# Kernel optimization log

Hardware: AMD Instinct MI355X
Metric: run time of the kernel (lower is better)

The kernel has to match this reference:

```python
import jax, jax.numpy as jnp
import numpy as np

HEADS = 8
DIM_HEAD = 64
SCALE = DIM_HEAD ** -0.5


def setup_inputs() -> dict:
    key = jax.random.key(0)
    ks = jax.random.split(key, 5)
    dim, hidden = 512, HEADS * DIM_HEAD
    b, l = 4, 2048
    return {
        "x": jax.random.normal(ks[0], (b, dim, l), jnp.float32),
        "w_qkv": jax.random.normal(ks[1], (3 * hidden, dim), jnp.float32) * 0.02,
        "b_qkv": jax.random.normal(ks[2], (3 * hidden,), jnp.float32) * 0.02,
        "w_out": jax.random.normal(ks[3], (dim, hidden), jnp.float32) * 0.02,
        "b_out": jax.random.normal(ks[4], (dim,), jnp.float32) * 0.02,
    }


def reference(x, w_qkv, b_qkv, w_out, b_out):
    b, c, l = x.shape
    # Conv1d kernel-size-1 == per-position linear: (b, 3*hidden, l)
    qkv = jnp.einsum('oc,bcl->bol', w_qkv, x) + b_qkv[None, :, None]
    q, k, v = jnp.split(qkv, 3, axis=1)
    # rearrange 'b (h d) l -> b h d l'
    def split_heads(t):
        return t.reshape(b, HEADS, DIM_HEAD, l)
    q, k, v = split_heads(q) * SCALE, split_heads(k), split_heads(v)
    sim = jnp.einsum('bhdi,bhdj->bhij', q, k)  # [b,h,l,l]
    sim = sim - jax.lax.stop_gradient(jnp.max(sim, axis=-1, keepdims=True))
    attn = jax.nn.softmax(sim, axis=-1)
    out = jnp.einsum('bhij,bhdj->bhid', attn, v)  # [b,h,l,d]
    # 'b h l d -> b (h d) l'
    out = out.transpose(0, 1, 3, 2).reshape(b, HEADS * DIM_HEAD, l)
    out = jnp.einsum('oc,bcl->bol', w_out, out) + b_out[None, :, None]
    return out
```

## Files before the change

kernel.cpp:

```cpp
#include <hip/hip_runtime.h>
#include <hip/hip_bf16.h>

#define B 4
#define DIM 512
#define HID 512
#define NH 8
#define DH 64
#define L 2048
#define SCALE 0.125f

typedef __attribute__((ext_vector_type(8)))  short bf16x8;
typedef __attribute__((ext_vector_type(4)))  float f32x4;
typedef __attribute__((ext_vector_type(16))) float f32x16;
typedef __attribute__((ext_vector_type(4)))  int   i32x4;

static __device__ __forceinline__ short f32_to_bf16s(float f) {
    __hip_bfloat16 h = __float2bfloat16(f);
    return *reinterpret_cast<short*>(&h);
}
static __device__ __forceinline__ float bf16s_to_f32(short s) {
    return __uint_as_float(((unsigned)(unsigned short)s) << 16);
}

static __device__ __forceinline__ void gl_lds16(const short* g, short* l) {
    __builtin_amdgcn_global_load_lds(
        (const __attribute__((address_space(1))) void*)g,
        (__attribute__((address_space(3))) void*)l, 16, 0, 0);
}

static __device__ __forceinline__ bf16x8 lds_frag(const short* t, int row, int c) {
    bf16x8 v;
    __builtin_memcpy(&v, t + row * 64 + ((c ^ (row & 7)) * 8), 16);
    return v;
}

__global__ __launch_bounds__(256) void prep_w(
    const float* __restrict__ wq, const float* __restrict__ wo,
    short* __restrict__ dst)
{
    const int g = blockIdx.x * 256 + threadIdx.x;
    const int i = g * 4;
    float4 v;
    if (i < 786432) v = *(const float4*)(wq + i);
    else            v = *(const float4*)(wo + (i - 786432));
    short4 pk = {f32_to_bf16s(v.x), f32_to_bf16s(v.y),
                 f32_to_bf16s(v.z), f32_to_bf16s(v.w)};
    *(short4*)(dst + i) = pk;
}

__global__ __launch_bounds__(256) void transpose_x(
    const float* __restrict__ X, short* __restrict__ XT)
{
    const int l0 = blockIdx.x * 64;
    const int c0 = blockIdx.y * 64;
    const int b  = blockIdx.z;
    const int tid = threadIdx.x;

    __shared__ float tile[64][65];
    const float* Xb = X + (size_t)b * DIM * L;

    #pragma unroll
    for (int it = 0; it < 16; ++it) {
        const int cr = (tid >> 6) + it * 4;
        const int lc = tid & 63;
        tile[cr][lc] = Xb[(size_t)(c0 + cr) * L + l0 + lc];
    }
    __syncthreads();
    short* XTb = XT + (size_t)b * L * DIM;
    #pragma unroll
    for (int it = 0; it < 8; ++it) {
        const int l  = (tid >> 5) + it * 8;
        const int c2 = (tid & 31) * 2;
        short2 pk = {f32_to_bf16s(tile[c2][l]), f32_to_bf16s(tile[c2 + 1][l])};
        *(short2*)(XTb + (size_t)(l0 + l) * DIM + c0 + c2) = pk;
    }
}

__global__ __launch_bounds__(256) void qkv_mfma(
    const short* __restrict__ Wb, const short* __restrict__ XT,
    const float* __restrict__ bias,
    short* __restrict__ qws, short* __restrict__ kws, short* __restrict__ vws)
{
    const int lBase = blockIdx.x * 128;
    const int oBase = blockIdx.y * 128;
    const int b     = blockIdx.z;
    const int tid   = threadIdx.x;
    const int wave  = tid >> 6;
    const int lane  = tid & 63;
    const int lid   = lane & 15;
    const int quad  = lane >> 4;
    const int rsub  = lane >> 3;
    const int cl    = (lane & 7) ^ rsub;

    __shared__ __align__(16) short Wt[128 * 64];
    __shared__ __align__(16) short Xt[128 * 64];

    const short* XTb = XT + (size_t)b * L * DIM;
    const int oLoc = (wave & 1) * 64;
    const int lLoc = (wave >> 1) * 64;

    f32x4 acc[4][4];
    #pragma unroll
    for (int mi = 0; mi < 4; ++mi)
        #pragma unroll
        for (int ni = 0; ni < 4; ++ni) acc[mi][ni] = (f32x4){0.f, 0.f, 0.f, 0.f};

    for (int c0 = 0; c0 < DIM; c0 += 64) {
        if (c0) __syncthreads();
        #pragma unroll
        for (int t = 0; t < 4; ++t) {
            const int ch = wave * 4 + t;
            const int r  = ch * 8 + rsub;
            gl_lds16(Wb  + (size_t)(oBase + r) * DIM + c0 + cl * 8, Wt + ch * 512);
            gl_lds16(XTb + (size_t)(lBase + r) * DIM + c0 + cl * 8, Xt + ch * 512);
        }
        __syncthreads();
        #pragma unroll
        for (int kc = 0; kc < 2; ++kc) {
            bf16x8 a[4], bb[4];
            #pragma unroll
            for (int mi = 0; mi < 4; ++mi)
                a[mi] = lds_frag(Wt, oLoc + mi * 16 + lid, kc * 4 + quad);
            #pragma unroll
            for (int ni = 0; ni < 4; ++ni)
                bb[ni] = lds_frag(Xt, lLoc + ni * 16 + lid, kc * 4 + quad);
            #pragma unroll
            for (int mi = 0; mi < 4; ++mi)
                #pragma unroll
                for (int ni = 0; ni < 4; ++ni)
                    acc[mi][ni] = __builtin_amdgcn_mfma_f32_16x16x32_bf16(
                        a[mi], bb[ni], acc[mi][ni], 0, 0, 0);
        }
    }

    const int rty = oBase >> 9;
    const float sc = (rty == 0) ? SCALE : 1.0f;
    const int h = ((oBase + oLoc) >> 6) & 7;

    #pragma unroll
    for (int mi = 0; mi < 4; ++mi) {
        const int dB = mi * 16 + quad * 4;
        float bia[4];
        #pragma unroll
        for (int r = 0; r < 4; ++r)
            bia[r] = bias[oBase + oLoc + mi * 16 + quad * 4 + r];

        if (rty < 2) {
            short* dst = (rty == 0 ? qws : kws) + (((size_t)b * NH + h) * L) * DH;
            #pragma unroll
            for (int ni = 0; ni < 4; ++ni) {
                const int l = lBase + lLoc + ni * 16 + lid;
                short4 pk = {f32_to_bf16s((acc[mi][ni][0] + bia[0]) * sc),
                             f32_to_bf16s((acc[mi][ni][1] + bia[1]) * sc),
                             f32_to_bf16s((acc[mi][ni][2] + bia[2]) * sc),
                             f32_to_bf16s((acc[mi][ni][3] + bia[3]) * sc)};
                *(short4*)(dst + (size_t)l * DH + dB) = pk;
            }
        } else {
            short* dst = vws + (((size_t)b * NH + h) * DH) * L;
            #pragma unroll
            for (int r = 0; r < 4; ++r) {
                const int d = dB + r;
                #pragma unroll
                for (int ni = 0; ni < 4; ++ni)
                    dst[(size_t)d * L + lBase + lLoc + ni * 16 + lid] =
                        f32_to_bf16s((acc[mi][ni][r] + bia[r]) * sc);
            }
        }
    }
}

__global__ __launch_bounds__(256) void attn_mfma(
    const short* __restrict__ Q, const short* __restrict__ K,
    const short* __restrict__ VT,
    float* __restrict__ Op0, float* __restrict__ Op1,
    float* __restrict__ Lp0, float* __restrict__ Lp1)
{
    const int iTile = blockIdx.x;
    const int h     = blockIdx.y;
    const int b     = blockIdx.z >> 1;
    const int half  = blockIdx.z & 1;
    const int tid   = threadIdx.x;
    const int wave  = tid >> 6;
    const int lane  = tid & 63;
    const int l5    = lane & 31;
    const int me    = lane >> 5;
    const int rsub  = lane >> 3;
    const int cl    = (lane & 7) ^ rsub;

    float* __restrict__ Op = half ? Op1 : Op0;
    float* __restrict__ Lp = half ? Lp1 : Lp0;

    const size_t headOff = ((size_t)b * NH + h) * (size_t)L * DH;
    const short* Qh = Q + headOff;
    const short* Kh = K + headOff;
    const short* Vh = VT + headOff;

    __shared__ __align__(16) short Kt[64 * 64];
    __shared__ __align__(16) short Vt[64 * 64];

    const int q0 = iTile * 128 + wave * 32;
    bf16x8 qf[4];
    #pragma unroll
    for (int kc = 0; kc < 4; ++kc)
        qf[kc] = *(const bf16x8*)(Qh + (size_t)(q0 + l5) * DH + kc * 16 + me * 8);

    f32x16 oacc[2];
    #pragma unroll
    for (int dt = 0; dt < 2; ++dt)
        #pragma unroll
        for (int r = 0; r < 16; ++r) oacc[dt][r] = 0.f;
    float lsum = 0.f;

    const int jt0 = half * 16;
    for (int jt = jt0; jt < jt0 + 16; ++jt) {
        const int j0 = jt * 64;
        if (jt > jt0) __syncthreads();
        #pragma unroll
        for (int t = 0; t < 2; ++t) {
            const int ch = wave * 2 + t;
            const int r  = ch * 8 + rsub;
            gl_lds16(Kh + (size_t)(j0 + r) * DH + cl * 8, Kt + ch * 512);
            gl_lds16(Vh + (size_t)r * L + j0 + cl * 8,    Vt + ch * 512);
        }
        __syncthreads();

        bf16x8 pf[4];
        #pragma unroll
        for (int mt = 0; mt < 2; ++mt) {
            f32x16 s;
            #pragma unroll
            for (int r = 0; r < 16; ++r) s[r] = 0.f;
            #pragma unroll
            for (int kc = 0; kc < 4; ++kc) {
                bf16x8 a = lds_frag(Kt, mt * 32 + l5, kc * 2 + me);
                s = __builtin_amdgcn_mfma_f32_32x32x16_bf16(a, qf[kc], s, 0, 0, 0);
            }
            unsigned short pbs[16];
            #pragma unroll
            for (int r = 0; r < 16; ++r) {
                float p = __expf(s[r]);
                unsigned short pb = (unsigned short)f32_to_bf16s(p);
                pbs[r] = pb;
                lsum += bf16s_to_f32((short)pb);
            }
            unsigned dw[4][2];
            #pragma unroll
            for (int g = 0; g < 4; ++g) {
                dw[g][0] = (unsigned)pbs[4 * g] | ((unsigned)pbs[4 * g + 1] << 16);
                dw[g][1] = (unsigned)pbs[4 * g + 2] | ((unsigned)pbs[4 * g + 3] << 16);
            }
            #pragma unroll
            for (int kl = 0; kl < 2; ++kl) {
                const unsigned own0 = me ? dw[2 * kl + 1][0] : dw[2 * kl][0];
                const unsigned own1 = me ? dw[2 * kl + 1][1] : dw[2 * kl][1];
                const unsigned snd0 = me ? dw[2 * kl][0] : dw[2 * kl + 1][0];
                const unsigned snd1 = me ? dw[2 * kl][1] : dw[2 * kl + 1][1];
                const unsigned rcv0 = (unsigned)__shfl_xor((int)snd0, 32);
                const unsigned rcv1 = (unsigned)__shfl_xor((int)snd1, 32);
                i32x4 bi;
                bi[0] = (int)(me ? rcv0 : own0);
                bi[1] = (int)(me ? rcv1 : own1);
                bi[2] = (int)(me ? own0 : rcv0);
                bi[3] = (int)(me ? own1 : rcv1);
                pf[mt * 2 + kl] = __builtin_bit_cast(bf16x8, bi);
            }
        }

        #pragma unroll
        for (int kc = 0; kc < 4; ++kc) {
            #pragma unroll
            for (int dt = 0; dt < 2; ++dt) {
                bf16x8 a = lds_frag(Vt, dt * 32 + l5, kc * 2 + me);
                oacc[dt] = __builtin_amdgcn_mfma_f32_32x32x16_bf16(a, pf[kc], oacc[dt], 0, 0, 0);
            }
        }
    }

    {
        float v = lsum + __shfl_xor(lsum, 32);
        if (me == 0)
            Lp[((size_t)b * NH + h) * L + q0 + l5] = v;
    }

    const int qg = q0 + l5;
    #pragma unroll
    for (int dt = 0; dt < 2; ++dt) {
        #pragma unroll
        for (int g = 0; g < 4; ++g) {
            const int d = dt * 32 + 8 * g + 4 * me;
            float4 v = {oacc[dt][4 * g], oacc[dt][4 * g + 1],
                        oacc[dt][4 * g + 2], oacc[dt][4 * g + 3]};
            *(float4*)(Op + ((size_t)b * L + qg) * HID + h * DH + d) = v;
        }
    }
}

__global__ __launch_bounds__(256) void combine(
    const float* __restrict__ Op0, const float* __restrict__ Op1,
    const float* __restrict__ Lp0, const float* __restrict__ Lp1,
    short* __restrict__ Abf)
{
    const int g = blockIdx.x * 256 + threadIdx.x;
    const int i = g * 4;
    const int b = i >> 20;
    const int rem = i & 1048575;
    const int l = rem >> 9;
    const int c = rem & 511;
    const int h = c >> 6;
    const size_t li = ((size_t)b * NH + h) * L + l;
    const float inv = 1.0f / (Lp0[li] + Lp1[li]);
    const float4 o0 = *(const float4*)(Op0 + i);
    const float4 o1 = *(const float4*)(Op1 + i);
    short4 pk = {f32_to_bf16s((o0.x + o1.x) * inv),
                 f32_to_bf16s((o0.y + o1.y) * inv),
                 f32_to_bf16s((o0.z + o1.z) * inv),
                 f32_to_bf16s((o0.w + o1.w) * inv)};
    *(short4*)(Abf + i) = pk;
}

__global__ __launch_bounds__(256) void out_mfma(
    const short* __restrict__ Wo, const short* __restrict__ Abf,
    const float* __restrict__ bias, float* __restrict__ out)
{
    const int lBase = blockIdx.x * 128;
    const int oBase = blockIdx.y * 64;
    const int b     = blockIdx.z;
    const int tid   = threadIdx.x;
    const int wave  = tid >> 6;
    const int lane  = tid & 63;
    const int lid   = lane & 15;
    const int quad  = lane >> 4;
    const int rsub  = lane >> 3;
    const int cl    = (lane & 7) ^ rsub;

    __shared__ __align__(16) short Wt[64 * 64];
    __shared__ __align__(16) short At[128 * 64];

    const short* Ab = Abf + (size_t)b * L * HID;
    const int oLoc = (wave & 1) * 32;
    const int lLoc = (wave >> 1) * 64;

    f32x4 acc[2][4];
    #pragma unroll
    for (int mi = 0; mi < 2; ++mi)
        #pragma unroll
        for (int ni = 0; ni < 4; ++ni) acc[mi][ni] = (f32x4){0.f, 0.f, 0.f, 0.f};

    for (int c0 = 0; c0 < HID; c0 += 64) {
        if (c0) __syncthreads();
        #pragma unroll
        for (int t = 0; t < 2; ++t) {
            const int ch = wave * 2 + t;
            const int r  = ch * 8 + rsub;
            gl_lds16(Wo + (size_t)(oBase + r) * HID + c0 + cl * 8, Wt + ch * 512);
        }
        #pragma unroll
        for (int t = 0; t < 4; ++t) {
            const int ch = wave * 4 + t;
            const int r  = ch * 8 + rsub;
            gl_lds16(Ab + (size_t)(lBase + r) * HID + c0 + cl * 8, At + ch * 512);
        }
        __syncthreads();
        #pragma unroll
        for (int kc = 0; kc < 2; ++kc) {
            bf16x8 a[2], bb[4];
            #pragma unroll
            for (int mi = 0; mi < 2; ++mi)
                a[mi] = lds_frag(Wt, oLoc + mi * 16 + lid, kc * 4 + quad);
            #pragma unroll
            for (int ni = 0; ni < 4; ++ni)
                bb[ni] = lds_frag(At, lLoc + ni * 16 + lid, kc * 4 + quad);
            #pragma unroll
            for (int mi = 0; mi < 2; ++mi)
                #pragma unroll
                for (int ni = 0; ni < 4; ++ni)
                    acc[mi][ni] = __builtin_amdgcn_mfma_f32_16x16x32_bf16(
                        a[mi], bb[ni], acc[mi][ni], 0, 0, 0);
        }
    }

    #pragma unroll
    for (int mi = 0; mi < 2; ++mi) {
        #pragma unroll
        for (int r = 0; r < 4; ++r) {
            const int o = oBase + oLoc + mi * 16 + quad * 4 + r;
            const float bia = bias[o];
            #pragma unroll
            for (int ni = 0; ni < 4; ++ni)
                out[((size_t)b * DIM + o) * L + lBase + lLoc + ni * 16 + lid] =
                    acc[mi][ni][r] + bia;
        }
    }
}

extern "C" void kernel_launch(void* const* d_in, const int* in_sizes, int n_in,
                              void* d_out, int out_size, void* d_ws, size_t ws_size,
                              hipStream_t stream)
{
    const float* x     = (const float*)d_in[0];
    const float* w_qkv = (const float*)d_in[1];
    const float* b_qkv = (const float*)d_in[2];
    const float* w_out = (const float*)d_in[3];
    const float* b_out = (const float*)d_in[4];
    float* out = (float*)d_out;

    char* w = (char*)d_ws;
    short* xT  = (short*)(w);
    short* wqb = (short*)(w + (8u << 20));
    short* wob = wqb + 786432;
    short* qws = (short*)(w + (10u << 20));
    short* kws = (short*)(w + (18u << 20));
    short* vws = (short*)(w + (26u << 20));
    short* Abf = (short*)(w + (34u << 20));
    float* Op1 = (float*)(w + (42u << 20));
    float* Lp0 = (float*)(w + (58u << 20));
    float* Lp1 = Lp0 + (size_t)B * NH * L;
    float* Op0 = out;

    dim3 blk(256);
    prep_w<<<dim3(1024), blk, 0, stream>>>(w_qkv, w_out, wqb);
    transpose_x<<<dim3(L / 64, DIM / 64, B), blk, 0, stream>>>(x, xT);
    qkv_mfma<<<dim3(L / 128, 1536 / 128, B), blk, 0, stream>>>(
        wqb, xT, b_qkv, qws, kws, vws);
    attn_mfma<<<dim3(L / 128, NH, B * 2), blk, 0, stream>>>(
        qws, kws, vws, Op0, Op1, Lp0, Lp1);
    combine<<<dim3(4096), blk, 0, stream>>>(Op0, Op1, Lp0, Lp1, Abf);
    out_mfma<<<dim3(L / 128, DIM / 64, B), blk, 0, stream>>>(
        wob, Abf, b_out, out);
}
```

Measured before the change: 176.1 us.

## Fuse split-KV combine into attention block via LDS reduction, use exp2 softmax

The two KV halves move from separate blocks into two wave groups of one 512-thread block, and the partial outputs are reduced through shared memory. The normalised bf16 output is written directly, which removes the fp32 partial buffers and the separate combine kernel launch. The softmax now uses exp2 with log2e folded into the Q scale, and bf16 packing is done by mask truncation instead of round-to-nearest, which changes rounding slightly. Grid block count halves while the block size doubles, and launch bounds now ask for 6 waves per SIMD.

Measured after the change: 223.5 us. 26.9% more time.

```diff
diff --git a/kernel.cpp b/kernel.cpp
--- a/kernel.cpp
+++ b/kernel.cpp
@@ -7,7 +7,7 @@
 #define NH 8
 #define DH 64
 #define L 2048
-#define SCALE 0.125f
+#define QSCALE (0.125f * 1.4426950408889634f)
 
 typedef __attribute__((ext_vector_type(8)))  short bf16x8;
 typedef __attribute__((ext_vector_type(4)))  float f32x4;
@@ -17,9 +17,6 @@
 static __device__ __forceinline__ short f32_to_bf16s(float f) {
     __hip_bfloat16 h = __float2bfloat16(f);
     return *reinterpret_cast<short*>(&h);
-}
-static __device__ __forceinline__ float bf16s_to_f32(short s) {
-    return __uint_as_float(((unsigned)(unsigned short)s) << 16);
 }
 
 static __device__ __forceinline__ void gl_lds16(const short* g, short* l) {
@@ -134,7 +131,7 @@
     }
 
     const int rty = oBase >> 9;
-    const float sc = (rty == 0) ? SCALE : 1.0f;
+    const float sc = (rty == 0) ? QSCALE : 1.0f;
     const int h = ((oBase + oLoc) >> 6) & 7;
 
     #pragma unroll
@@ -170,36 +167,35 @@
     }
 }
 
-__global__ __launch_bounds__(256) void attn_mfma(
+__global__ __launch_bounds__(512, 6) void attn_mfma(
     const short* __restrict__ Q, const short* __restrict__ K,
-    const short* __restrict__ VT,
-    float* __restrict__ Op0, float* __restrict__ Op1,
-    float* __restrict__ Lp0, float* __restrict__ Lp1)
+    const short* __restrict__ VT, short* __restrict__ Abf)
 {
     const int iTile = blockIdx.x;
     const int h     = blockIdx.y;
-    const int b     = blockIdx.z >> 1;
-    const int half  = blockIdx.z & 1;
+    const int b     = blockIdx.z;
     const int tid   = threadIdx.x;
     const int wave  = tid >> 6;
+    const int half  = wave >> 2;
+    const int w4    = wave & 3;
     const int lane  = tid & 63;
     const int l5    = lane & 31;
     const int me    = lane >> 5;
     const int rsub  = lane >> 3;
     const int cl    = (lane & 7) ^ rsub;
 
-    float* __restrict__ Op = half ? Op1 : Op0;
-    float* __restrict__ Lp = half ? Lp1 : Lp0;
-
     const size_t headOff = ((size_t)b * NH + h) * (size_t)L * DH;
     const short* Qh = Q + headOff;
     const short* Kh = K + headOff;
     const short* Vh = VT + headOff;
 
-    __shared__ __align__(16) short Kt[64 * 64];
-    __shared__ __align__(16) short Vt[64 * 64];
-
-    const int q0 = iTile * 128 + wave * 32;
+    __shared__ __align__(16) char smem[35328];
+    short* Kt = (short*)smem + half * 8192;
+    short* Vt = Kt + 4096;
+    float* OxF = (float*)smem;
+    float* LsX = (float*)(smem + 34816);
+
+    const int q0 = iTile * 128 + w4 * 32;
     bf16x8 qf[4];
     #pragma unroll
     for (int kc = 0; kc < 4; ++kc)
@@ -213,12 +209,12 @@
     float lsum = 0.f;
 
     const int jt0 = half * 16;
-    for (int jt = jt0; jt < jt0 + 16; ++jt) {
-        const int j0 = jt * 64;
-        if (jt > jt0) __syncthreads();
+    for (int it = 0; it < 16; ++it) {
+        const int j0 = (jt0 + it) * 64;
+        if (it) __syncthreads();
         #pragma unroll
         for (int t = 0; t < 2; ++t) {
-            const int ch = wave * 2 + t;
+            const int ch = w4 * 2 + t;
             const int r  = ch * 8 + rsub;
             gl_lds16(Kh + (size_t)(j0 + r) * DH + cl * 8, Kt + ch * 512);
             gl_lds16(Vh + (size_t)r * L + j0 + cl * 8,    Vt + ch * 512);
@@ -236,19 +232,18 @@
                 bf16x8 a = lds_frag(Kt, mt * 32 + l5, kc * 2 + me);
                 s = __builtin_amdgcn_mfma_f32_32x32x16_bf16(a, qf[kc], s, 0, 0, 0);
             }
-            unsigned short pbs[16];
-            #pragma unroll
-            for (int r = 0; r < 16; ++r) {
-                float p = __expf(s[r]);
-                unsigned short pb = (unsigned short)f32_to_bf16s(p);
-                pbs[r] = pb;
-                lsum += bf16s_to_f32((short)pb);
-            }
             unsigned dw[4][2];
             #pragma unroll
             for (int g = 0; g < 4; ++g) {
-                dw[g][0] = (unsigned)pbs[4 * g] | ((unsigned)pbs[4 * g + 1] << 16);
-                dw[g][1] = (unsigned)pbs[4 * g + 2] | ((unsigned)pbs[4 * g + 3] << 16);
+                #pragma unroll
+                for (int p = 0; p < 2; ++p) {
+                    const float p0 = exp2f(s[4 * g + 2 * p]);
+                    const float p1 = exp2f(s[4 * g + 2 * p + 1]);
+                    const unsigned u0 = __float_as_uint(p0) & 0xffff0000u;
+                    const unsigned u1 = __float_as_uint(p1) & 0xffff0000u;
+                    lsum += __uint_as_float(u0) + __uint_as_float(u1);
+                    dw[g][p] = (u0 >> 16) | u1;
+                }
             }
             #pragma unroll
             for (int kl = 0; kl < 2; ++kl) {
@@ -277,46 +272,39 @@
         }
     }
 
-    {
-        float v = lsum + __shfl_xor(lsum, 32);
-        if (me == 0)
-            Lp[((size_t)b * NH + h) * L + q0 + l5] = v;
-    }
-
-    const int qg = q0 + l5;
-    #pragma unroll
-    for (int dt = 0; dt < 2; ++dt) {
-        #pragma unroll
-        for (int g = 0; g < 4; ++g) {
-            const int d = dt * 32 + 8 * g + 4 * me;
-            float4 v = {oacc[dt][4 * g], oacc[dt][4 * g + 1],
-                        oacc[dt][4 * g + 2], oacc[dt][4 * g + 3]};
-            *(float4*)(Op + ((size_t)b * L + qg) * HID + h * DH + d) = v;
-        }
-    }
-}
-
-__global__ __launch_bounds__(256) void combine(
-    const float* __restrict__ Op0, const float* __restrict__ Op1,
-    const float* __restrict__ Lp0, const float* __restrict__ Lp1,
-    short* __restrict__ Abf)
-{
-    const int g = blockIdx.x * 256 + threadIdx.x;
-    const int i = g * 4;
-    const int b = i >> 20;
-    const int rem = i & 1048575;
-    const int l = rem >> 9;
-    const int c = rem & 511;
-    const int h = c >> 6;
-    const size_t li = ((size_t)b * NH + h) * L + l;
-    const float inv = 1.0f / (Lp0[li] + Lp1[li]);
-    const float4 o0 = *(const float4*)(Op0 + i);
-    const float4 o1 = *(const float4*)(Op1 + i);
-    short4 pk = {f32_to_bf16s((o0.x + o1.x) * inv),
-                 f32_to_bf16s((o0.y + o1.y) * inv),
-                 f32_to_bf16s((o0.z + o1.z) * inv),
-                 f32_to_bf16s((o0.w + o1.w) * inv)};
-    *(short4*)(Abf + i) = pk;
+    const float vh = lsum + __shfl_xor(lsum, 32);
+
+    __syncthreads();
+    if (half == 1) {
+        float* dst = OxF + w4 * (32 * 68) + l5 * 68;
+        #pragma unroll
+        for (int dt = 0; dt < 2; ++dt)
+            #pragma unroll
+            for (int g = 0; g < 4; ++g) {
+                float4 v = {oacc[dt][4 * g],     oacc[dt][4 * g + 1],
+                            oacc[dt][4 * g + 2], oacc[dt][4 * g + 3]};
+                *(float4*)(dst + dt * 32 + g * 8 + me * 4) = v;
+            }
+        if (me == 0) LsX[w4 * 32 + l5] = vh;
+    }
+    __syncthreads();
+    if (half == 0) {
+        const float inv = 1.0f / (vh + LsX[w4 * 32 + l5]);
+        const float* src = OxF + w4 * (32 * 68) + l5 * 68;
+        short* ab = Abf + ((size_t)b * L + q0 + l5) * HID + h * DH;
+        #pragma unroll
+        for (int dt = 0; dt < 2; ++dt)
+            #pragma unroll
+            for (int g = 0; g < 4; ++g) {
+                const float4 o1 = *(const float4*)(src + dt * 32 + g * 8 + me * 4);
+                short4 pk = {
+                    f32_to_bf16s((oacc[dt][4 * g]     + o1.x) * inv),
+                    f32_to_bf16s((oacc[dt][4 * g + 1] + o1.y) * inv),
+                    f32_to_bf16s((oacc[dt][4 * g + 2] + o1.z) * inv),
+                    f32_to_bf16s((oacc[dt][4 * g + 3] + o1.w) * inv)};
+                *(short4*)(ab + dt * 32 + g * 8 + me * 4) = pk;
+            }
+    }
 }
 
 __global__ __launch_bounds__(256) void out_mfma(
@@ -413,19 +401,14 @@
     short* kws = (short*)(w + (18u << 20));
     short* vws = (short*)(w + (26u << 20));
     short* Abf = (short*)(w + (34u << 20));
-    float* Op1 = (float*)(w + (42u << 20));
-    float* Lp0 = (float*)(w + (58u << 20));
-    float* Lp1 = Lp0 + (size_t)B * NH * L;
-    float* Op0 = out;
 
     dim3 blk(256);
     prep_w<<<dim3(1024), blk, 0, stream>>>(w_qkv, w_out, wqb);
     transpose_x<<<dim3(L / 64, DIM / 64, B), blk, 0, stream>>>(x, xT);
     qkv_mfma<<<dim3(L / 128, 1536 / 128, B), blk, 0, stream>>>(
         wqb, xT, b_qkv, qws, kws, vws);
-    attn_mfma<<<dim3(L / 128, NH, B * 2), blk, 0, stream>>>(
-        qws, kws, vws, Op0, Op1, Lp0, Lp1);
-    combine<<<dim3(4096), blk, 0, stream>>>(Op0, Op1, Lp0, Lp1, Abf);
+    attn_mfma<<<dim3(L / 128, NH, B), dim3(512), 0, stream>>>(
+        qws, kws, vws, Abf);
     out_mfma<<<dim3(L / 128, DIM / 64, B), blk, 0, stream>>>(
         wob, Abf, b_out, out);
 }
```
